# Kernel optimization log

Measured on AMD Instinct MI355X. Metric: run time of the kernel, lower is better.

Reference implementation:

```python
import jax, jax.numpy as jnp
import numpy as np

B, C, H, W = 4, 256, 64, 64
CQK = C // 8  # 32


def setup_inputs() -> dict:
    key = jax.random.key(0)
    ks = jax.random.split(key, 8)
    s = 0.05
    return {
        "x": jax.random.normal(ks[0], (B, C, H, W), dtype=jnp.float32),
        "wq": jax.random.normal(ks[1], (CQK, C), dtype=jnp.float32) * s,
        "bq": jax.random.normal(ks[2], (CQK,), dtype=jnp.float32) * s,
        "wk": jax.random.normal(ks[3], (CQK, C), dtype=jnp.float32) * s,
        "bk": jax.random.normal(ks[4], (CQK,), dtype=jnp.float32) * s,
        "wv": jax.random.normal(ks[5], (C, C), dtype=jnp.float32) * s,
        "bv": jax.random.normal(ks[6], (C,), dtype=jnp.float32) * s,
        "gamma": jax.random.normal(ks[7], (1,), dtype=jnp.float32),
    }


def reference(x, wq, bq, wk, bk, wv, bv, gamma):
    b, c, h, w = x.shape
    n = h * w
    xf = x.reshape(b, c, n)  # (B, C, N)
    # 1x1 conv + bias + ReLU (Conv2d wrapper default activate='relu')
    q = jax.nn.relu(jnp.einsum('oc,bcn->bon', wq, xf) + bq[:, None])  # (B, CQK, N)
    k = jax.nn.relu(jnp.einsum('oc,bcn->bon', wk, xf) + bk[:, None])  # (B, CQK, N)
    v = jax.nn.relu(jnp.einsum('oc,bcn->bon', wv, xf) + bv[:, None])  # (B, C, N)
    # energy[b, i, j] = sum_c q[b, c, i] * k[b, c, j]
    energy = jnp.einsum('bci,bcj->bij', q, k)  # (B, N, N)
    attention = jax.nn.softmax(energy, axis=-1)
    # out[b, c, i] = sum_j v[b, c, j] * attention[b, i, j]
    out = jnp.einsum('bcj,bij->bci', v, attention)  # (B, C, N)
    out = out.reshape(b, c, h, w)
    return gamma[0] * out + x
```

## Files before the change

### kernel.cpp

```cpp
#include <hip/hip_runtime.h>
#include <stdint.h>


#define NB 4
#define CD 256
#define ND 4096
#define CQ 32
#define LOG2E 1.4426950408889634f

typedef __attribute__((ext_vector_type(4))) float f32x4;
typedef __attribute__((ext_vector_type(8))) _Float16 f16x8;
typedef __attribute__((ext_vector_type(4))) unsigned short u16x4;
typedef __attribute__((ext_vector_type(8))) unsigned short u16x8;
typedef __attribute__((ext_vector_type(2))) unsigned int u32x2;
typedef __attribute__((ext_vector_type(4))) unsigned int u32x4;
typedef __attribute__((ext_vector_type(4))) int i32x4;

static __device__ __forceinline__ unsigned short f2h(float f) {
    union { _Float16 h; unsigned short u; } cv; cv.h = (_Float16)f; return cv.u;
}
static __device__ __forceinline__ float h2f(unsigned short u) {
    union { unsigned short u; _Float16 h; } cv; cv.u = u; return (float)cv.h;
}
static __device__ __forceinline__ float fexp2(float xv) {
    float r; asm("v_exp_f32 %0, %1" : "=v"(r) : "v"(xv)); return r;
}

__global__ __launch_bounds__(256) void wcvt_kernel(
    const float* __restrict__ wq, const float* __restrict__ wk,
    const float* __restrict__ wv, unsigned short* __restrict__ Wh)
{
    const int idx = blockIdx.x * 256 + threadIdx.x;
    const int m = idx >> 6, kq = (idx & 63) << 2;
    const float* src = (m < 32) ? (wq + (size_t)m * CD + kq)
                     : (m < 64) ? (wk + (size_t)(m - 32) * CD + kq)
                                : (wv + (size_t)(m - 64) * CD + kq);
    const f32x4 v = *reinterpret_cast<const f32x4*>(src);
    u16x4 h;
#pragma unroll
    for (int u = 0; u < 4; ++u) h[u] = f2h(v[u]);
    *reinterpret_cast<u16x4*>(Wh + (size_t)m * CD + kq) = h;
}

__global__ __launch_bounds__(640) void proj_kernel(
    const float* __restrict__ x, const unsigned short* __restrict__ Wh,
    const float* __restrict__ bq, const float* __restrict__ bk,
    const float* __restrict__ bv,
    unsigned short* __restrict__ Qt, unsigned short* __restrict__ Kt,
    unsigned short* __restrict__ Vp)
{
    __shared__ __align__(16) unsigned char xls[64 * 512];

    const int tid = threadIdx.x;
    const int lane = tid & 63;
    const int w = __builtin_amdgcn_readfirstlane(tid >> 6);
    const int m16 = lane & 15, g4 = lane >> 4;
    const int b = blockIdx.x >> 6, n0 = (blockIdx.x & 63) << 6;

    {
        const float* xb = x + (size_t)b * CD * ND + n0;
#pragma unroll 1
        for (int idx = tid; idx < 4096; idx += 640) {
            const int c = idx >> 4, nq = (idx & 15) << 2;
            const f32x4 v = *reinterpret_cast<const f32x4*>(xb + (size_t)c * ND + nq);
#pragma unroll
            for (int r = 0; r < 4; ++r) {
                const int row = nq + r;
                const int ad = (row * 512 + c * 2) ^ ((row & 7) << 4);
                *reinterpret_cast<unsigned short*>(&xls[ad]) = f2h(v[r]);
            }
        }
    }
    __syncthreads();

    f32x4 acc[2][4];
#pragma unroll
    for (int a = 0; a < 2; ++a)
#pragma unroll
        for (int c = 0; c < 4; ++c) acc[a][c] = (f32x4){0.f, 0.f, 0.f, 0.f};

    const unsigned short* Wrow = Wh + (size_t)(w * 32 + m16) * CD;
    const int bswz = (m16 & 7) << 4;
    const bool qk = (w < 2);

#pragma unroll
    for (int ks = 0; ks < 8; ++ks) {
        const int ko = ks * 32 + g4 * 8;
        f16x8 af[2], bf[4];
#pragma unroll
        for (int ms = 0; ms < 2; ++ms)
            af[ms] = *reinterpret_cast<const f16x8*>(Wrow + (size_t)ms * 16 * CD + ko);
#pragma unroll
        for (int ns = 0; ns < 4; ++ns) {
            const int ad = ((ns * 16 + m16) * 512 + ko * 2) ^ bswz;
            bf[ns] = *reinterpret_cast<const f16x8*>(&xls[ad]);
        }
        if (qk) {
#pragma unroll
            for (int ms = 0; ms < 2; ++ms)
#pragma unroll
                for (int ns = 0; ns < 4; ++ns)
                    acc[ms][ns] = __builtin_amdgcn_mfma_f32_16x16x32_f16(
                        af[ms], bf[ns], acc[ms][ns], 0, 0, 0);
        } else {
#pragma unroll
            for (int ms = 0; ms < 2; ++ms)
#pragma unroll
                for (int ns = 0; ns < 4; ++ns)
                    acc[ms][ns] = __builtin_amdgcn_mfma_f32_16x16x32_f16(
                        bf[ns], af[ms], acc[ms][ns], 0, 0, 0);
        }
    }

    if (w == 0) {
#pragma unroll
        for (int ms = 0; ms < 2; ++ms) {
            const int mb = ms * 16 + g4 * 4;
            const f32x4 bias = *reinterpret_cast<const f32x4*>(bq + mb);
#pragma unroll
            for (int ns = 0; ns < 4; ++ns) {
                const int n = n0 + ns * 16 + m16;
                u16x4 h;
#pragma unroll
                for (int r = 0; r < 4; ++r)
                    h[r] = f2h(fmaxf(acc[ms][ns][r] + bias[r], 0.f) * LOG2E);
                *reinterpret_cast<u16x4*>(Qt + ((size_t)(b * ND + n)) * CQ + mb) = h;
            }
        }
    } else if (w == 1) {
#pragma unroll
        for (int ms = 0; ms < 2; ++ms) {
            const int mb = ms * 16 + g4 * 4;
            const f32x4 bias = *reinterpret_cast<const f32x4*>(bk + mb);
#pragma unroll
            for (int ns = 0; ns < 4; ++ns) {
                const int n = n0 + ns * 16 + m16;
                u16x4 h;
#pragma unroll
                for (int r = 0; r < 4; ++r)
                    h[r] = f2h(fmaxf(acc[ms][ns][r] + bias[r], 0.f));
                *reinterpret_cast<u16x4*>(Kt + ((size_t)(b * ND + n)) * CQ + mb) = h;
            }
        }
    } else {
        const int cbase = (w - 2) * 32;
#pragma unroll
        for (int ms = 0; ms < 2; ++ms) {
            const int c = cbase + ms * 16 + m16;
            const float bval = bv[c];
#pragma unroll
            for (int ns = 0; ns < 4; ++ns) {
                const int n = n0 + ns * 16 + g4 * 4;
                u16x4 h;
#pragma unroll
                for (int r = 0; r < 4; ++r)
                    h[r] = f2h(fmaxf(acc[ms][ns][r] + bval, 0.f));
                unsigned short* dst = Vp
                    + ((size_t)((b * 128 + (n >> 5)) * 16 + (c >> 4))) * 512
                    + ((((n >> 3) & 3) * 16 + (c & 15)) * 8) + (n & 7);
                *reinterpret_cast<u16x4*>(dst) = h;
            }
        }
    }
}

__global__ __launch_bounds__(512, 2) void attn_kernel(
    const unsigned short* __restrict__ Qt, const unsigned short* __restrict__ Kt,
    const unsigned short* __restrict__ Vp,
    unsigned short* __restrict__ OpH, float* __restrict__ Mb, float* __restrict__ Lb)
{
    __shared__ __align__(16) unsigned char smem[68096];
    __shared__ int gctr[2];
    float* scales = reinterpret_cast<float*>(smem + 32768);
    int*   flags  = reinterpret_cast<int*>(smem + 34816);
    float* Ocomb  = reinterpret_cast<float*>(smem);
    float* mfin   = reinterpret_cast<float*>(smem + 66560);
    float* lfin   = reinterpret_cast<float*>(smem + 67072);
    float* wfac   = reinterpret_cast<float*>(smem + 67584);

    const int tid  = threadIdx.x;
    const int lane = tid & 63;
    const int w8   = __builtin_amdgcn_readfirstlane(tid >> 6);
    const int g    = w8 >> 2;
    const int ws   = w8 & 3;
    const int m16  = lane & 15;
    const int g4   = lane >> 4;
    const int wg   = (blockIdx.x & 7) * 64 + (blockIdx.x >> 3);
    const int jh   = wg >> 8;
    const int b    = (wg >> 6) & 3;
    const int i0   = (wg & 63) << 6;

    if (tid < 2) gctr[tid] = 0;
    __syncthreads();

    const f16x8 qfrag = *reinterpret_cast<const f16x8*>(
        Qt + ((size_t)(b * ND + i0 + ws * 16 + m16)) * CQ + g4 * 8);
    const unsigned short* kb = Kt + ((size_t)(b * ND + m16)) * CQ + g4 * 8;
    const unsigned short* vpc =
        Vp + ((size_t)(b * 128 * 16 + ws * 4)) * 512 + lane * 8;

    f32x4 oacc[4][4];
#pragma unroll
    for (int a = 0; a < 4; ++a)
#pragma unroll
        for (int c = 0; c < 4; ++c) oacc[a][c] = (f32x4){0.f, 0.f, 0.f, 0.f};
    float mrow = -1e30f;
    float lrow = 0.f;
    const f32x4 zero4 = {0.f, 0.f, 0.f, 0.f};

    const int jbase = jh * 2048 + g * 1024;
    const int irow  = ws * 16 + m16;
    const int iswz  = (m16 & 7) << 4;

    auto LOADK = [&](f16x8 (&kr)[4], int j) {
#pragma unroll
        for (int t = 0; t < 4; ++t)
            kr[t] = *reinterpret_cast<const f16x8*>(kb + (size_t)(j + t * 16) * CQ);
    };

    auto GSYNC = [&](int k) {
        asm volatile("s_waitcnt lgkmcnt(0)" ::: "memory");
        if (lane == 0) atomicAdd(&gctr[g], 1);
        const int tgt = (k + 1) * 4;
        int cv = __builtin_amdgcn_readfirstlane(*(volatile int*)&gctr[g]);
        while (cv < tgt) {
            __builtin_amdgcn_s_sleep(1);
            cv = __builtin_amdgcn_readfirstlane(*(volatile int*)&gctr[g]);
        }
    };

    auto STEP = [&](int k, f16x8 (&kc)[4], f16x8 (&kn)[4]) {
        const int j0  = jbase + k * 64;
        const int par = k & 1;
        unsigned char* pb = smem + g * 16384 + par * 8192;

        const int jblk0 = j0 >> 5;
        f16x8 vf[2][4];
#pragma unroll
        for (int jhh = 0; jhh < 2; ++jhh)
#pragma unroll
            for (int cs = 0; cs < 4; ++cs)
                vf[jhh][cs] = *reinterpret_cast<const f16x8*>(
                    vpc + (size_t)((jblk0 + jhh) * 16 + cs) * 512);
        const int jn = (k < 15) ? (j0 + 64) : jbase;
        LOADK(kn, jn);

        f32x4 sv[4];
#pragma unroll
        for (int t = 0; t < 4; ++t)
            sv[t] = __builtin_amdgcn_mfma_f32_16x16x32_f16(kc[t], qfrag, zero4, 0, 0, 0);

        float pm = sv[0][0];
#pragma unroll
        for (int t = 0; t < 4; ++t)
#pragma unroll
            for (int r = 0; r < 4; ++r) pm = fmaxf(pm, sv[t][r]);
        float sc = 1.0f;
        int myresc = 0;
        if (__ballot(pm <= mrow + 8.0f) != ~0ull) {
            float pr = fmaxf(pm, __shfl_xor(pm, 16));
            pr = fmaxf(pr, __shfl_xor(pr, 32));
            const float mnew = fmaxf(mrow, pr);
            sc = fexp2(mrow - mnew);
            mrow = mnew;
            myresc = 1;
        }
        float rs = 0.f;
#pragma unroll
        for (int t = 0; t < 4; ++t)
#pragma unroll
            for (int r = 0; r < 4; ++r) { sv[t][r] = fexp2(sv[t][r] - mrow); rs += sv[t][r]; }
        lrow = lrow * sc + rs;

#pragma unroll
        for (int t = 0; t < 4; ++t) {
            u32x2 pw;
            pw[0] = __builtin_bit_cast(unsigned int,
                        __builtin_amdgcn_cvt_pkrtz(sv[t][0], sv[t][1]));
            pw[1] = __builtin_bit_cast(unsigned int,
                        __builtin_amdgcn_cvt_pkrtz(sv[t][2], sv[t][3]));
            const int lo = (irow * 128 + t * 32 + g4 * 8) ^ iswz;
            *reinterpret_cast<u32x2*>(pb + lo) = pw;
        }
        if (g4 == 0)   scales[(g * 2 + par) * 64 + irow] = sc;
        if (lane == 0) flags[(g * 2 + par) * 4 + ws] = myresc;

        GSYNC(k);

        const i32x4 fl = *reinterpret_cast<const i32x4*>(flags + (g * 2 + par) * 4);
        const int anyresc = __builtin_amdgcn_readfirstlane(fl[0] | fl[1] | fl[2] | fl[3]);
        if (anyresc) {
#pragma unroll
            for (int is = 0; is < 4; ++is) {
                const f32x4 sr = *reinterpret_cast<const f32x4*>(
                    scales + (g * 2 + par) * 64 + is * 16 + g4 * 4);
#pragma unroll
                for (int r = 0; r < 4; ++r)
#pragma unroll
                    for (int cs = 0; cs < 4; ++cs) oacc[is][cs][r] *= sr[r];
            }
        }

        __builtin_amdgcn_s_setprio(1);
#pragma unroll
        for (int jhh = 0; jhh < 2; ++jhh) {
#pragma unroll
            for (int is = 0; is < 4; ++is) {
                const int lo = ((is * 16 + m16) * 128 + jhh * 64 + g4 * 16) ^ iswz;
                const f16x8 pf = *reinterpret_cast<const f16x8*>(pb + lo);
#pragma unroll
                for (int cs = 0; cs < 4; ++cs)
                    oacc[is][cs] = __builtin_amdgcn_mfma_f32_16x16x32_f16(
                        pf, vf[jhh][cs], oacc[is][cs], 0, 0, 0);
            }
        }
        __builtin_amdgcn_s_setprio(0);
    };

    f16x8 kA[4], kB[4];
    LOADK(kA, jbase);

#pragma unroll 1
    for (int k2 = 0; k2 < 8; ++k2) {
        STEP(2 * k2,     kA, kB);
        STEP(2 * k2 + 1, kB, kA);
    }

    lrow += __shfl_xor(lrow, 16);
    lrow += __shfl_xor(lrow, 32);
    if (g4 == 0) { mfin[g * 64 + irow] = mrow; lfin[g * 64 + irow] = lrow; }
    __syncthreads();

    if (tid < 128) {
        const int gg = tid >> 6, i = tid & 63;
        const float m0 = mfin[i], m1 = mfin[64 + i];
        const float M  = fmaxf(m0, m1);
        const float e  = fexp2(((gg == 0) ? m0 : m1) - M);
        wfac[gg * 64 + i] = e;
        if (gg == 0) {
            const float e1 = fexp2(m1 - M);
            Mb[(size_t)wg * 64 + i] = M;
            Lb[(size_t)wg * 64 + i] = lfin[i] * fexp2(m0 - M) + lfin[64 + i] * e1;
        }
    }
    __syncthreads();

    if (g == 0) {
#pragma unroll
        for (int is = 0; is < 4; ++is) {
            const f32x4 f = *reinterpret_cast<const f32x4*>(wfac + is * 16 + g4 * 4);
#pragma unroll
            for (int cs = 0; cs < 4; ++cs)
#pragma unroll
                for (int r = 0; r < 4; ++r)
                    Ocomb[(is * 16 + g4 * 4 + r) * 260 + ws * 64 + cs * 16 + m16] =
                        oacc[is][cs][r] * f[r];
        }
    }
    __syncthreads();
    if (g == 1) {
#pragma unroll
        for (int is = 0; is < 4; ++is) {
            const f32x4 f = *reinterpret_cast<const f32x4*>(wfac + 64 + is * 16 + g4 * 4);
#pragma unroll
            for (int cs = 0; cs < 4; ++cs)
#pragma unroll
                for (int r = 0; r < 4; ++r)
                    Ocomb[(is * 16 + g4 * 4 + r) * 260 + ws * 64 + cs * 16 + m16] +=
                        oacc[is][cs][r] * f[r];
        }
    }
    __syncthreads();

#pragma unroll
    for (int pass = 0; pass < 4; ++pass) {
        const int q = tid + pass * 512;
        const int c = q >> 3, i8 = (q & 7) * 8;
        u32x4 o;
#pragma unroll
        for (int u = 0; u < 4; ++u)
            o[u] = __builtin_bit_cast(unsigned int,
                       __builtin_amdgcn_cvt_pkrtz(Ocomb[(i8 + 2 * u) * 260 + c],
                                                  Ocomb[(i8 + 2 * u + 1) * 260 + c]));
        *reinterpret_cast<u32x4*>(OpH + ((size_t)wg * 256 + c) * 64 + i8) = o;
    }
}

__global__ __launch_bounds__(256) void combine_kernel(
    const unsigned short* __restrict__ OpH, const float* __restrict__ Mb,
    const float* __restrict__ Lb, const float* __restrict__ x,
    const float* __restrict__ gamma, float* __restrict__ out)
{
    __shared__ float w0[64], w1[64];
    const int tid = threadIdx.x;
    const int pb  = blockIdx.x;
    const int b   = pb >> 6, istrip = pb & 63;
    const int wg0 = pb, wg1 = 256 + pb;

    if (tid < 64) {
        const float m0 = Mb[(size_t)wg0 * 64 + tid], m1 = Mb[(size_t)wg1 * 64 + tid];
        const float l0 = Lb[(size_t)wg0 * 64 + tid], l1 = Lb[(size_t)wg1 * 64 + tid];
        const float M  = fmaxf(m0, m1);
        const float e0 = fexp2(m0 - M), e1 = fexp2(m1 - M);
        const float den = l0 * e0 + l1 * e1;
        w0[tid] = e0 / den;
        w1[tid] = e1 / den;
    }
    __syncthreads();

    const float gm = gamma[0];
#pragma unroll 1
    for (int pass = 0; pass < 8; ++pass) {
        const int q = tid + pass * 256;
        const int c = q >> 3, i8 = (q & 7) * 8;
        const u16x8 o0 = *reinterpret_cast<const u16x8*>(
            OpH + ((size_t)wg0 * 256 + c) * 64 + i8);
        const u16x8 o1 = *reinterpret_cast<const u16x8*>(
            OpH + ((size_t)wg1 * 256 + c) * 64 + i8);
        const size_t idx = ((size_t)(b * CD + c)) * ND + istrip * 64 + i8;
        const f32x4 xa = *reinterpret_cast<const f32x4*>(x + idx);
        const f32x4 xb2 = *reinterpret_cast<const f32x4*>(x + idx + 4);
        f32x4 ra, rb;
#pragma unroll
        for (int u = 0; u < 4; ++u) {
            const float v0 = h2f(o0[u]) * w0[i8 + u] + h2f(o1[u]) * w1[i8 + u];
            const float v1 = h2f(o0[u + 4]) * w0[i8 + u + 4] + h2f(o1[u + 4]) * w1[i8 + u + 4];
            ra[u] = gm * v0 + xa[u];
            rb[u] = gm * v1 + xb2[u];
        }
        *reinterpret_cast<f32x4*>(out + idx)     = ra;
        *reinterpret_cast<f32x4*>(out + idx + 4) = rb;
    }
}

extern "C" void kernel_launch(void* const* d_in, const int* in_sizes, int n_in,
                              void* d_out, int out_size, void* d_ws, size_t ws_size,
                              hipStream_t stream) {
    const float* x     = (const float*)d_in[0];
    const float* wq    = (const float*)d_in[1];
    const float* bq    = (const float*)d_in[2];
    const float* wk    = (const float*)d_in[3];
    const float* bk    = (const float*)d_in[4];
    const float* wv    = (const float*)d_in[5];
    const float* bv    = (const float*)d_in[6];
    const float* gamma = (const float*)d_in[7];

    unsigned short* Qt  = (unsigned short*)d_ws;
    unsigned short* Kt  = Qt + (size_t)NB * ND * CQ;
    unsigned short* Vp  = Kt + (size_t)NB * ND * CQ;
    unsigned short* Wh  = Vp + (size_t)NB * CD * ND;
    unsigned short* OpH = Wh + (size_t)320 * CD;
    float* Mb = (float*)(OpH + (size_t)512 * 256 * 64);
    float* Lb = Mb + (size_t)512 * 64;
    float* out = (float*)d_out;

    wcvt_kernel<<<dim3(80),      dim3(256), 0, stream>>>(wq, wk, wv, Wh);
    proj_kernel<<<dim3(NB * 64), dim3(640), 0, stream>>>(x, Wh, bq, bk, bv, Qt, Kt, Vp);
    attn_kernel<<<dim3(512),     dim3(512), 0, stream>>>(Qt, Kt, Vp, OpH, Mb, Lb);
    combine_kernel<<<dim3(256),  dim3(256), 0, stream>>>(OpH, Mb, Lb, x, gamma, out);
}
```

Measured before the change: 82.25 us.

## Combine partial attention outputs in fp16 LDS and store directly from registers

The epilogue no longer stages the combined output in a float LDS buffer with a transposed read pass. Group 0 writes normalized fp16 partials into a compact fp16 LDS tile, and group 1 adds its own partials and stores straight to global memory. This drops one barrier and roughly halves LDS use, which may allow more blocks per CU. The per-half outputs are now pre-normalized by their own L, so the combine kernel weights by l*e/den. The cost is extra fp16 rounding of the intermediate and narrower 8-byte global stores.

```diff
diff --git a/kernel.cpp b/kernel.cpp
--- a/kernel.cpp
+++ b/kernel.cpp
@@ -13,7 +13,6 @@
 typedef __attribute__((ext_vector_type(4))) unsigned short u16x4;
 typedef __attribute__((ext_vector_type(8))) unsigned short u16x8;
 typedef __attribute__((ext_vector_type(2))) unsigned int u32x2;
-typedef __attribute__((ext_vector_type(4))) unsigned int u32x4;
 typedef __attribute__((ext_vector_type(4))) int i32x4;
 
 static __device__ __forceinline__ unsigned short f2h(float f) {
@@ -24,6 +23,9 @@
 }
 static __device__ __forceinline__ float fexp2(float xv) {
     float r; asm("v_exp_f32 %0, %1" : "=v"(r) : "v"(xv)); return r;
+}
+static __device__ __forceinline__ unsigned int pk2(float a, float b) {
+    return __builtin_bit_cast(unsigned int, __builtin_amdgcn_cvt_pkrtz(a, b));
 }
 
 __global__ __launch_bounds__(256) void wcvt_kernel(
@@ -169,14 +171,13 @@
     const unsigned short* __restrict__ Vp,
     unsigned short* __restrict__ OpH, float* __restrict__ Mb, float* __restrict__ Lb)
 {
-    __shared__ __align__(16) unsigned char smem[68096];
+    __shared__ __align__(16) unsigned char smem[36416];
     __shared__ int gctr[2];
     float* scales = reinterpret_cast<float*>(smem + 32768);
     int*   flags  = reinterpret_cast<int*>(smem + 34816);
-    float* Ocomb  = reinterpret_cast<float*>(smem);
-    float* mfin   = reinterpret_cast<float*>(smem + 66560);
-    float* lfin   = reinterpret_cast<float*>(smem + 67072);
-    float* wfac   = reinterpret_cast<float*>(smem + 67584);
+    float* mfin   = reinterpret_cast<float*>(smem + 34880);
+    float* lfin   = reinterpret_cast<float*>(smem + 35392);
+    float* wfac   = reinterpret_cast<float*>(smem + 35904);
 
     const int tid  = threadIdx.x;
     const int lane = tid & 63;
@@ -275,10 +276,8 @@
 #pragma unroll
         for (int t = 0; t < 4; ++t) {
             u32x2 pw;
-            pw[0] = __builtin_bit_cast(unsigned int,
-                        __builtin_amdgcn_cvt_pkrtz(sv[t][0], sv[t][1]));
-            pw[1] = __builtin_bit_cast(unsigned int,
-                        __builtin_amdgcn_cvt_pkrtz(sv[t][2], sv[t][3]));
+            pw[0] = pk2(sv[t][0], sv[t][1]);
+            pw[1] = pk2(sv[t][2], sv[t][3]);
             const int lo = (irow * 128 + t * 32 + g4 * 8) ^ iswz;
             *reinterpret_cast<u32x2*>(pb + lo) = pw;
         }
@@ -331,30 +330,32 @@
     if (g4 == 0) { mfin[g * 64 + irow] = mrow; lfin[g * 64 + irow] = lrow; }
     __syncthreads();
 
-    if (tid < 128) {
-        const int gg = tid >> 6, i = tid & 63;
-        const float m0 = mfin[i], m1 = mfin[64 + i];
+    if (tid < 64) {
+        const float m0 = mfin[tid], m1 = mfin[64 + tid];
         const float M  = fmaxf(m0, m1);
-        const float e  = fexp2(((gg == 0) ? m0 : m1) - M);
-        wfac[gg * 64 + i] = e;
-        if (gg == 0) {
-            const float e1 = fexp2(m1 - M);
-            Mb[(size_t)wg * 64 + i] = M;
-            Lb[(size_t)wg * 64 + i] = lfin[i] * fexp2(m0 - M) + lfin[64 + i] * e1;
-        }
-    }
-    __syncthreads();
-
+        const float e0 = fexp2(m0 - M), e1 = fexp2(m1 - M);
+        const float Lv = lfin[tid] * e0 + lfin[64 + tid] * e1;
+        Mb[(size_t)wg * 64 + tid] = M;
+        Lb[(size_t)wg * 64 + tid] = Lv;
+        const float rinv = 1.0f / Lv;
+        wfac[tid]      = e0 * rinv;
+        wfac[64 + tid] = e1 * rinv;
+    }
+    __syncthreads();
+
+    unsigned short* Oc = reinterpret_cast<unsigned short*>(smem);
     if (g == 0) {
 #pragma unroll
         for (int is = 0; is < 4; ++is) {
             const f32x4 f = *reinterpret_cast<const f32x4*>(wfac + is * 16 + g4 * 4);
 #pragma unroll
-            for (int cs = 0; cs < 4; ++cs)
-#pragma unroll
-                for (int r = 0; r < 4; ++r)
-                    Ocomb[(is * 16 + g4 * 4 + r) * 260 + ws * 64 + cs * 16 + m16] =
-                        oacc[is][cs][r] * f[r];
+            for (int cs = 0; cs < 4; ++cs) {
+                const int c = ws * 64 + cs * 16 + m16;
+                u32x2 pw;
+                pw[0] = pk2(oacc[is][cs][0] * f[0], oacc[is][cs][1] * f[1]);
+                pw[1] = pk2(oacc[is][cs][2] * f[2], oacc[is][cs][3] * f[3]);
+                *reinterpret_cast<u32x2*>(&Oc[c * 68 + is * 16 + g4 * 4]) = pw;
+            }
         }
     }
     __syncthreads();
@@ -363,26 +364,21 @@
         for (int is = 0; is < 4; ++is) {
             const f32x4 f = *reinterpret_cast<const f32x4*>(wfac + 64 + is * 16 + g4 * 4);
 #pragma unroll
-            for (int cs = 0; cs < 4; ++cs)
-#pragma unroll
-                for (int r = 0; r < 4; ++r)
-                    Ocomb[(is * 16 + g4 * 4 + r) * 260 + ws * 64 + cs * 16 + m16] +=
-                        oacc[is][cs][r] * f[r];
-        }
-    }
-    __syncthreads();
-
-#pragma unroll
-    for (int pass = 0; pass < 4; ++pass) {
-        const int q = tid + pass * 512;
-        const int c = q >> 3, i8 = (q & 7) * 8;
-        u32x4 o;
-#pragma unroll
-        for (int u = 0; u < 4; ++u)
-            o[u] = __builtin_bit_cast(unsigned int,
-                       __builtin_amdgcn_cvt_pkrtz(Ocomb[(i8 + 2 * u) * 260 + c],
-                                                  Ocomb[(i8 + 2 * u + 1) * 260 + c]));
-        *reinterpret_cast<u32x4*>(OpH + ((size_t)wg * 256 + c) * 64 + i8) = o;
+            for (int cs = 0; cs < 4; ++cs) {
+                const int c = ws * 64 + cs * 16 + m16;
+                const u32x2 prev = *reinterpret_cast<const u32x2*>(
+                    &Oc[c * 68 + is * 16 + g4 * 4]);
+                const float q0 = h2f((unsigned short)(prev[0] & 0xffff));
+                const float q1 = h2f((unsigned short)(prev[0] >> 16));
+                const float q2 = h2f((unsigned short)(prev[1] & 0xffff));
+                const float q3 = h2f((unsigned short)(prev[1] >> 16));
+                u32x2 pw;
+                pw[0] = pk2(q0 + oacc[is][cs][0] * f[0], q1 + oacc[is][cs][1] * f[1]);
+                pw[1] = pk2(q2 + oacc[is][cs][2] * f[2], q3 + oacc[is][cs][3] * f[3]);
+                *reinterpret_cast<u32x2*>(
+                    OpH + ((size_t)wg * 256 + c) * 64 + is * 16 + g4 * 4) = pw;
+            }
+        }
     }
 }
 
@@ -403,8 +399,8 @@
         const float M  = fmaxf(m0, m1);
         const float e0 = fexp2(m0 - M), e1 = fexp2(m1 - M);
         const float den = l0 * e0 + l1 * e1;
-        w0[tid] = e0 / den;
-        w1[tid] = e1 / den;
+        w0[tid] = l0 * e0 / den;
+        w1[tid] = l1 * e1 / den;
     }
     __syncthreads();
 
```

Measured after the change: 80.80 us. About the same (-1.8%).
